# Kernel tuning notes

Hardware: AMD Instinct MI355X
Metric: run time of the kernel (lower is better)

## Reference

```python
import jax, jax.numpy as jnp
import numpy as np

U, I, H, E, EL = 100000, 50000, 128, 600000, 200000


def setup_inputs() -> dict:
    key = jax.random.key(0)
    ks = jax.random.split(key, 24)
    inp = {}
    inp["user_emb"] = jax.random.normal(ks[0], (U, H), jnp.float32) * 0.1
    inp["item_emb"] = jax.random.normal(ks[1], (I, H), jnp.float32) * 0.1
    s = 1.0 / np.sqrt(H)
    names = ["w1_ui_l", "w1_ui_r", "w1_iu_l", "w1_iu_r",
             "w2_ui_l", "w2_ui_r", "w2_iu_l", "w2_iu_r"]
    for i, n in enumerate(names):
        inp[n] = jax.random.uniform(ks[2 + i], (H, H), jnp.float32, -s, s)
    for i, n in enumerate(["b1_ui", "b1_iu", "b2_ui", "b2_iu"]):
        inp[n] = jax.random.uniform(ks[10 + i], (H,), jnp.float32, -s, s)
    inp["user_node_id"] = jnp.arange(U, dtype=jnp.int32)
    inp["item_node_id"] = jnp.arange(I, dtype=jnp.int32)
    src_u = jax.random.randint(ks[14], (E,), 0, U, jnp.int32)
    dst_i = jax.random.randint(ks[15], (E,), 0, I, jnp.int32)
    inp["edge_index_ui"] = jnp.stack([src_u, dst_i])  # user -> item
    inp["edge_index_iu"] = jnp.stack([dst_i, src_u])  # item -> user (reverse)
    lu = jax.random.randint(ks[16], (EL,), 0, U, jnp.int32)
    li = jax.random.randint(ks[17], (EL,), 0, I, jnp.int32)
    inp["edge_label_index"] = jnp.stack([lu, li])
    return inp


def _sage(x_src, x_dst, edge_index, w_l, b_l, w_r, num_dst):
    # PyG SAGEConv: out = lin_l(mean_j x_src[j]) + lin_r(x_dst)
    src, dst = edge_index[0], edge_index[1]
    msg = x_src[src]                                   # [E, H] gather
    agg = jax.ops.segment_sum(msg, dst, num_segments=num_dst)
    cnt = jax.ops.segment_sum(jnp.ones((msg.shape[0],), msg.dtype), dst,
                              num_segments=num_dst)
    mean = agg / jnp.maximum(cnt, 1.0)[:, None]
    return mean @ w_l + b_l + x_dst @ w_r


def reference(user_emb, item_emb,
              w1_ui_l, w1_ui_r, w1_iu_l, w1_iu_r,
              w2_ui_l, w2_ui_r, w2_iu_l, w2_iu_r,
              b1_ui, b1_iu, b2_ui, b2_iu,
              user_node_id, item_node_id,
              edge_index_ui, edge_index_iu, edge_label_index):
    xu = user_emb[user_node_id]   # [U, H]
    xi = item_emb[item_node_id]   # [I, H]
    # layer 1 (hetero: each dst type aggregates from its single incoming relation)
    u1 = jax.nn.relu(_sage(xi, xu, edge_index_iu, w1_iu_l, b1_iu, w1_iu_r, U))
    i1 = jax.nn.relu(_sage(xu, xi, edge_index_ui, w1_ui_l, b1_ui, w1_ui_r, I))
    # layer 2
    u2 = _sage(i1, u1, edge_index_iu, w2_iu_l, b2_iu, w2_iu_r, U)
    i2 = _sage(u1, i1, edge_index_ui, w2_ui_l, b2_ui, w2_ui_r, I)
    # edge-indexed dot-product classifier
    fu = u2[edge_label_index[0]]  # [EL, H]
    fi = i2[edge_label_index[1]]  # [EL, H]
    return jnp.sum(fu * fi, axis=-1)
```

## Files before the change

kernel.cpp:

```cpp
#include <hip/hip_runtime.h>
#include <hip/hip_bf16.h>
#include <cstdio>

#define U_N 100000
#define I_N 50000
#define H_DIM 128
#define E_N 600000
#define EL_N 200000

#define EPB 2048
#define NBLK ((E_N + EPB - 1) / EPB)
#define SH_U 8
#define SH_I 7
#define NB_U ((U_N + 255) >> 8)
#define NB_I ((I_N + 127) >> 7)
#define LH_U (NB_U * NBLK)
#define LH_I (NB_I * NBLK)

#define NBLK_GU ((U_N + 127) / 128)
#define NBLK_GI ((I_N + 127) / 128)

typedef __attribute__((ext_vector_type(8))) short bh8;
typedef __attribute__((ext_vector_type(4))) float f32x4;
typedef __attribute__((ext_vector_type(8))) unsigned short u16x8;

__device__ inline unsigned short f2b(float f) {
  unsigned u = __builtin_bit_cast(unsigned, f);
  u += 0x7fffu + ((u >> 16) & 1u);
  return (unsigned short)(u >> 16);
}
__device__ inline float b2f(unsigned short h) {
  unsigned u = ((unsigned)h) << 16;
  return __builtin_bit_cast(float, u);
}

__global__ __launch_bounds__(256) void bin_hist(const int* __restrict__ dst,
                                                int* __restrict__ hist,
                                                int shift, int nbins) {
  __shared__ int h[512];
  const int t = threadIdx.x;
  for (int i = t; i < nbins; i += 256) h[i] = 0;
  __syncthreads();
  const int base = blockIdx.x * EPB;
  const int end = min(base + EPB, E_N);
  for (int i = base + t; i < end; i += 256)
    atomicAdd(&h[((unsigned)dst[i]) >> shift], 1);
  __syncthreads();
  for (int i = t; i < nbins; i += 256)
    hist[i * NBLK + blockIdx.x] = h[i];
}

__global__ __launch_bounds__(256) void bin_scatter(const int* __restrict__ dst,
                                                   const int* __restrict__ src,
                                                   const int* __restrict__ hoff,
                                                   unsigned* __restrict__ bucketed,
                                                   int shift, int nbins) {
  __shared__ int cur[512];
  const int t = threadIdx.x;
  for (int i = t; i < nbins; i += 256) cur[i] = hoff[i * NBLK + blockIdx.x];
  __syncthreads();
  const int base = blockIdx.x * EPB;
  const int end = min(base + EPB, E_N);
  const unsigned mask = (1u << shift) - 1u;
  for (int i = base + t; i < end; i += 256) {
    unsigned d = (unsigned)dst[i];
    int bin = (int)(d >> shift);
    int pos = atomicAdd(&cur[bin], 1);
    bucketed[pos] = ((d & mask) << 24) | (unsigned)src[i];
  }
}

__global__ __launch_bounds__(256) void bin_group(const int* __restrict__ hoff,
                                                 const unsigned* __restrict__ bucketed,
                                                 int* __restrict__ csr,
                                                 int* __restrict__ cnt,
                                                 int* __restrict__ off,
                                                 int shift, int nbins, int N) {
  __shared__ int cl[256];
  __shared__ int cur[256];
  __shared__ int wsum[4];
  const int b = blockIdx.x;
  const int t = threadIdx.x;
  const int start = hoff[b * NBLK];
  const int end = (b + 1 < nbins) ? hoff[(b + 1) * NBLK] : E_N;
  const int ndst = 1 << shift;
  const int base = b << shift;
  if (t < ndst) cl[t] = 0;
  __syncthreads();
  for (int i = start + t; i < end; i += 256)
    atomicAdd(&cl[bucketed[i] >> 24], 1);
  __syncthreads();
  int v = (t < ndst) ? cl[t] : 0;
  const int lane = t & 63, wv = t >> 6;
  int inc = v;
  for (int d = 1; d < 64; d <<= 1) {
    int x = __shfl_up(inc, d, 64);
    if (lane >= d) inc += x;
  }
  if (lane == 63) wsum[wv] = inc;
  __syncthreads();
  int wbase = 0;
  for (int q = 0; q < wv; ++q) wbase += wsum[q];
  int excl = wbase + inc - v;
  if (t < ndst) {
    cur[t] = start + excl;
    int node = base + t;
    if (node < N) { cnt[node] = v; off[node] = start + excl; }
  }
  __syncthreads();
  for (int i = start + t; i < end; i += 256) {
    unsigned w = bucketed[i];
    int pos = atomicAdd(&cur[w >> 24], 1);
    csr[pos] = (int)(w & 0xFFFFFFu);
  }
}

__global__ __launch_bounds__(256) void cvt_emb2(const float* __restrict__ xu,
                                                const float* __restrict__ xi,
                                                const int* __restrict__ unid,
                                                const int* __restrict__ inid,
                                                unsigned short* __restrict__ ub,
                                                unsigned short* __restrict__ ib) {
  int t = blockIdx.x * 256 + threadIdx.x;
  const float* x;
  unsigned short* xb;
  int row, seg;
  if (t < U_N * 16) {
    row = t >> 4; seg = t & 15;
    row = unid ? unid[row] : row;
    x = xu; xb = ub + ((size_t)(t >> 4)) * H_DIM;
  } else {
    int t2 = t - U_N * 16;
    if (t2 >= I_N * 16) return;
    row = t2 >> 4; seg = t2 & 15;
    int r0 = row;
    row = inid ? inid[row] : row;
    x = xi; xb = ib + (size_t)r0 * H_DIM;
  }
  const float* p = x + (size_t)row * H_DIM + seg * 8;
  float4 a = ((const float4*)p)[0];
  float4 b = ((const float4*)p)[1];
  u16x8 v;
  v[0] = f2b(a.x); v[1] = f2b(a.y); v[2] = f2b(a.z); v[3] = f2b(a.w);
  v[4] = f2b(b.x); v[5] = f2b(b.y); v[6] = f2b(b.z); v[7] = f2b(b.w);
  *(u16x8*)(xb + seg * 8) = v;
}

__global__ __launch_bounds__(256) void scan_p1(const int* __restrict__ cnt,
                                               int* __restrict__ bsum, int n) {
  const int t = threadIdx.x;
  const int base = blockIdx.x * 1024 + t * 4;
  int s = 0;
  for (int j = 0; j < 4; ++j) {
    int i = base + j;
    if (i < n) s += cnt[i];
  }
  for (int off = 32; off > 0; off >>= 1) s += __shfl_down(s, off, 64);
  __shared__ int wsum[4];
  if ((t & 63) == 0) wsum[t >> 6] = s;
  __syncthreads();
  if (t == 0) bsum[blockIdx.x] = wsum[0] + wsum[1] + wsum[2] + wsum[3];
}

__global__ __launch_bounds__(256) void scan_p2(int* __restrict__ bsum, int nb) {
  __shared__ int sm[256];
  const int t = threadIdx.x;
  int v = (t < nb) ? bsum[t] : 0;
  sm[t] = v;
  __syncthreads();
  for (int d = 1; d < 256; d <<= 1) {
    int x = (t >= d) ? sm[t - d] : 0;
    __syncthreads();
    sm[t] += x;
    __syncthreads();
  }
  if (t < nb) bsum[t] = sm[t] - v;
}

__global__ __launch_bounds__(256) void scan_p3(const int* __restrict__ cnt,
                                               const int* __restrict__ bsum,
                                               int* __restrict__ off, int n) {
  const int t = threadIdx.x;
  const int lane = t & 63, wv = t >> 6;
  const int base = blockIdx.x * 1024 + t * 4;
  int vals[4];
  int s = 0;
  for (int j = 0; j < 4; ++j) {
    int i = base + j;
    vals[j] = (i < n) ? cnt[i] : 0;
    s += vals[j];
  }
  int inc = s;
  for (int d = 1; d < 64; d <<= 1) {
    int x = __shfl_up(inc, d, 64);
    if (lane >= d) inc += x;
  }
  __shared__ int wsum[4];
  if (lane == 63) wsum[wv] = inc;
  __syncthreads();
  int wbase = 0;
  for (int w = 0; w < wv; ++w) wbase += wsum[w];
  int excl = wbase + (inc - s) + bsum[blockIdx.x];
  for (int j = 0; j < 4; ++j) {
    int i = base + j;
    if (i < n) off[i] = excl;
    excl += vals[j];
  }
}

__global__ __launch_bounds__(256) void gather_mean2(
    const int* __restrict__ off_u, const int* __restrict__ cnt_u,
    const int* __restrict__ csr_u, const unsigned short* __restrict__ xsrc_u,
    unsigned short* __restrict__ agg_u,
    const int* __restrict__ off_i, const int* __restrict__ cnt_i,
    const int* __restrict__ csr_i, const unsigned short* __restrict__ xsrc_i,
    unsigned short* __restrict__ agg_i) {
  long t = (long)blockIdx.x * 256 + threadIdx.x;
  int node = (int)(t >> 4);
  int lane = (int)(t & 15);
  const int* off; const int* cnt; const int* csr;
  const unsigned short* xb; unsigned short* aggb;
  if (node < U_N) {
    off = off_u; cnt = cnt_u; csr = csr_u; xb = xsrc_u; aggb = agg_u;
  } else {
    node -= U_N;
    if (node >= I_N) return;
    off = off_i; cnt = cnt_i; csr = csr_i; xb = xsrc_i; aggb = agg_i;
  }
  int o = off[node], c = cnt[node];
  float acc[8] = {};
  for (int j0 = 0; j0 < c; j0 += 16) {
    int nj = c - j0;
    if (nj > 16) nj = 16;
    int sidx = (lane < nj) ? csr[o + j0 + lane] : 0;
    int j = 0;
    for (; j + 4 <= nj; j += 4) {
      int s0 = __shfl(sidx, j + 0, 16);
      int s1 = __shfl(sidx, j + 1, 16);
      int s2 = __shfl(sidx, j + 2, 16);
      int s3 = __shfl(sidx, j + 3, 16);
      u16x8 v0 = *(const u16x8*)(xb + (size_t)s0 * H_DIM + lane * 8);
      u16x8 v1 = *(const u16x8*)(xb + (size_t)s1 * H_DIM + lane * 8);
      u16x8 v2 = *(const u16x8*)(xb + (size_t)s2 * H_DIM + lane * 8);
      u16x8 v3 = *(const u16x8*)(xb + (size_t)s3 * H_DIM + lane * 8);
      for (int k = 0; k < 8; ++k) acc[k] += b2f(v0[k]);
      for (int k = 0; k < 8; ++k) acc[k] += b2f(v1[k]);
      for (int k = 0; k < 8; ++k) acc[k] += b2f(v2[k]);
      for (int k = 0; k < 8; ++k) acc[k] += b2f(v3[k]);
    }
    for (; j < nj; ++j) {
      int s = __shfl(sidx, j, 16);
      u16x8 v = *(const u16x8*)(xb + (size_t)s * H_DIM + lane * 8);
      for (int k = 0; k < 8; ++k) acc[k] += b2f(v[k]);
    }
  }
  float inv = 1.0f / (float)(c > 0 ? c : 1);
  u16x8 r;
  for (int k = 0; k < 8; ++k) r[k] = f2b(acc[k] * inv);
  *(u16x8*)(aggb + (size_t)node * H_DIM + lane * 8) = r;
}

__global__ __launch_bounds__(256) void prep_w4(
    const float* __restrict__ l0, const float* __restrict__ r0, short* __restrict__ o0,
    const float* __restrict__ l1, const float* __restrict__ r1, short* __restrict__ o1,
    const float* __restrict__ l2, const float* __restrict__ r2, short* __restrict__ o2,
    const float* __restrict__ l3, const float* __restrict__ r3, short* __restrict__ o3) {
  int t = blockIdx.x * 256 + threadIdx.x;
  int set = t >> 15, s = t & 32767;
  const float *wl, *wr; short* W2;
  if (set == 0)      { wl = l0; wr = r0; W2 = o0; }
  else if (set == 1) { wl = l1; wr = r1; W2 = o1; }
  else if (set == 2) { wl = l2; wr = r2; W2 = o2; }
  else               { wl = l3; wr = r3; W2 = o3; }
  int col = s >> 8, k = s & 255;
  float v = (k < 128) ? wl[k * 128 + col] : wr[(k - 128) * 128 + col];
  W2[col * 256 + k] = (short)f2b(v);
}

__global__ __launch_bounds__(256) void sage_gemm2(
    const unsigned short* __restrict__ agg_u, const unsigned short* __restrict__ x_u,
    const short* __restrict__ W2_u, const float* __restrict__ bias_u,
    unsigned short* __restrict__ out_u,
    const unsigned short* __restrict__ agg_i, const unsigned short* __restrict__ x_i,
    const short* __restrict__ W2_i, const float* __restrict__ bias_i,
    unsigned short* __restrict__ out_i, int relu) {
  const unsigned short *aggb, *xb;
  const short* W2;
  const float* bias;
  unsigned short* outb;
  int N, blk;
  if (blockIdx.x < NBLK_GU) {
    aggb = agg_u; xb = x_u; W2 = W2_u; bias = bias_u; outb = out_u;
    N = U_N; blk = blockIdx.x;
  } else {
    aggb = agg_i; xb = x_i; W2 = W2_i; bias = bias_i; outb = out_i;
    N = I_N; blk = blockIdx.x - NBLK_GU;
  }

  __shared__ short wlds[128 * 256];
  const int tid = threadIdx.x;
  for (int c = tid; c < 4096; c += 256) {
    int col = c >> 5, g = c & 31;
    uint4 v = *(const uint4*)(W2 + col * 256 + g * 8);
    *(uint4*)(&wlds[col * 256 + ((g ^ (col & 15)) * 8)]) = v;
  }
  __syncthreads();

  const int lane = tid & 63;
  const int wave = tid >> 6;
  const int q = lane >> 4;
  const int n16 = lane & 15;
  const int rowbase = blk * 128 + wave * 32;

  const unsigned short* aptr[2];
  const unsigned short* xptr[2];
  for (int g = 0; g < 2; ++g) {
    int row = rowbase + g * 16 + n16;
    int rr = row < N ? row : 0;
    aptr[g] = aggb + (size_t)rr * H_DIM + q * 8;
    xptr[g] = xb + (size_t)rr * H_DIM + q * 8;
  }

  f32x4 acc[2][8] = {};

  for (int kt = 0; kt < 8; ++kt) {
    const int k0 = kt * 32;
    bh8 afrag[2];
    for (int g = 0; g < 2; ++g) {
      const unsigned short* p = (kt < 4) ? (aptr[g] + k0) : (xptr[g] + (k0 - 128));
      afrag[g] = *(const bh8*)(p);
    }
    const int swz = ((kt * 4 + q) ^ n16) * 8;
    for (int c = 0; c < 8; ++c) {
      bh8 b = *(const bh8*)(&wlds[(c * 16 + n16) * 256 + swz]);
      acc[0][c] = __builtin_amdgcn_mfma_f32_16x16x32_bf16(afrag[0], b, acc[0][c], 0, 0, 0);
      acc[1][c] = __builtin_amdgcn_mfma_f32_16x16x32_bf16(afrag[1], b, acc[1][c], 0, 0, 0);
    }
  }

  float bcol[8];
  for (int c = 0; c < 8; ++c) bcol[c] = bias[c * 16 + n16];

  for (int g = 0; g < 2; ++g) {
    for (int r = 0; r < 4; ++r) {
      int row = rowbase + g * 16 + q * 4 + r;
      if (row >= N) continue;
      for (int c = 0; c < 8; ++c) {
        float v = acc[g][c][r] + bcol[c];
        if (relu) v = v > 0.0f ? v : 0.0f;
        outb[(size_t)row * H_DIM + c * 16 + n16] = f2b(v);
      }
    }
  }
}

__global__ __launch_bounds__(256) void final_dot(const int* __restrict__ lbl,
                                                 const unsigned short* __restrict__ u2,
                                                 const unsigned short* __restrict__ i2,
                                                 float* __restrict__ out) {
  long t = (long)blockIdx.x * 256 + threadIdx.x;
  int e = (int)(t >> 4);
  if (e >= EL_N) return;
  int lane = (int)(t & 15);
  int lu = lbl[e];
  int li = lbl[EL_N + e];
  u16x8 a = *(const u16x8*)(u2 + (size_t)lu * H_DIM + lane * 8);
  u16x8 b = *(const u16x8*)(i2 + (size_t)li * H_DIM + lane * 8);
  float p = 0.f;
  for (int k = 0; k < 8; ++k) p += b2f(a[k]) * b2f(b[k]);
  for (int off = 8; off > 0; off >>= 1) p += __shfl_down(p, off, 16);
  if (lane == 0) out[e] = p;
}

extern "C" void kernel_launch(void* const* d_in, const int* in_sizes, int n_in,
                              void* d_out, int out_size, void* d_ws, size_t ws_size,
                              hipStream_t stream) {
  const float* user_emb = (const float*)d_in[0];
  const float* item_emb = (const float*)d_in[1];
  const float* w1_ui_l = (const float*)d_in[2];
  const float* w1_ui_r = (const float*)d_in[3];
  const float* w1_iu_l = (const float*)d_in[4];
  const float* w1_iu_r = (const float*)d_in[5];
  const float* w2_ui_l = (const float*)d_in[6];
  const float* w2_ui_r = (const float*)d_in[7];
  const float* w2_iu_l = (const float*)d_in[8];
  const float* w2_iu_r = (const float*)d_in[9];
  const float* b1_ui = (const float*)d_in[10];
  const float* b1_iu = (const float*)d_in[11];
  const float* b2_ui = (const float*)d_in[12];
  const float* b2_iu = (const float*)d_in[13];
  const int* unid = (const int*)d_in[14];
  const int* inid = (const int*)d_in[15];
  const int* e_ui = (const int*)d_in[16];
  const int* e_iu = (const int*)d_in[17];
  const int* elbl = (const int*)d_in[18];
  float* out = (float*)d_out;

  char* ws = (char*)d_ws;
  size_t o = 0;
  auto alloc = [&](size_t bytes) {
    char* p = ws + o;
    o = (o + bytes + 255) & ~(size_t)255;
    return p;
  };
  int* hist_u = (int*)alloc((size_t)LH_U * 4);
  int* hoff_u = (int*)alloc((size_t)LH_U * 4);
  int* hist_i = (int*)alloc((size_t)LH_I * 4);
  int* hoff_i = (int*)alloc((size_t)LH_I * 4);
  unsigned* bkt_u = (unsigned*)alloc((size_t)E_N * 4);
  unsigned* bkt_i = (unsigned*)alloc((size_t)E_N * 4);
  int* cnt_u = (int*)alloc((size_t)U_N * 4);
  int* cnt_i = (int*)alloc((size_t)I_N * 4);
  int* off_u = (int*)alloc((size_t)U_N * 4);
  int* off_i = (int*)alloc((size_t)I_N * 4);
  int* csr_u = (int*)alloc((size_t)E_N * 4);
  int* csr_i = (int*)alloc((size_t)E_N * 4);
  int* bsum_u = (int*)alloc(256 * 4);
  int* bsum_i = (int*)alloc(256 * 4);
  unsigned short* ue_b = (unsigned short*)alloc((size_t)U_N * H_DIM * 2);
  unsigned short* ie_b = (unsigned short*)alloc((size_t)I_N * H_DIM * 2);
  unsigned short* agg_u = (unsigned short*)alloc((size_t)U_N * H_DIM * 2);
  unsigned short* agg_i = (unsigned short*)alloc((size_t)I_N * H_DIM * 2);
  unsigned short* h1_u = (unsigned short*)alloc((size_t)U_N * H_DIM * 2);
  unsigned short* h1_i = (unsigned short*)alloc((size_t)I_N * H_DIM * 2);
  unsigned short* h2_u = (unsigned short*)alloc((size_t)U_N * H_DIM * 2);
  unsigned short* h2_i = (unsigned short*)alloc((size_t)I_N * H_DIM * 2);
  short* W2_1u = (short*)alloc(128 * 256 * 2);
  short* W2_1i = (short*)alloc(128 * 256 * 2);
  short* W2_2u = (short*)alloc(128 * 256 * 2);
  short* W2_2i = (short*)alloc(128 * 256 * 2);
  if (o > ws_size) {
    fprintf(stderr, "kernel_launch: ws too small, need %zu have %zu\n", o, ws_size);
    return;
  }

  cvt_emb2<<<((U_N + I_N) * 16 + 255) / 256, 256, 0, stream>>>(
      user_emb, item_emb, unid, inid, ue_b, ie_b);
  prep_w4<<<512, 256, 0, stream>>>(w1_iu_l, w1_iu_r, W2_1u,
                                   w1_ui_l, w1_ui_r, W2_1i,
                                   w2_iu_l, w2_iu_r, W2_2u,
                                   w2_ui_l, w2_ui_r, W2_2i);

  bin_hist<<<NBLK, 256, 0, stream>>>(e_ui, hist_u, SH_U, NB_U);
  bin_hist<<<NBLK, 256, 0, stream>>>(e_ui + E_N, hist_i, SH_I, NB_I);

  scan_p1<<<(LH_U + 1023) / 1024, 256, 0, stream>>>(hist_u, bsum_u, LH_U);
  scan_p1<<<(LH_I + 1023) / 1024, 256, 0, stream>>>(hist_i, bsum_i, LH_I);
  scan_p2<<<1, 256, 0, stream>>>(bsum_u, (LH_U + 1023) / 1024);
  scan_p2<<<1, 256, 0, stream>>>(bsum_i, (LH_I + 1023) / 1024);
  scan_p3<<<(LH_U + 1023) / 1024, 256, 0, stream>>>(hist_u, bsum_u, hoff_u, LH_U);
  scan_p3<<<(LH_I + 1023) / 1024, 256, 0, stream>>>(hist_i, bsum_i, hoff_i, LH_I);

  bin_scatter<<<NBLK, 256, 0, stream>>>(e_ui, e_ui + E_N, hoff_u, bkt_u, SH_U, NB_U);
  bin_scatter<<<NBLK, 256, 0, stream>>>(e_ui + E_N, e_ui, hoff_i, bkt_i, SH_I, NB_I);

  bin_group<<<NB_U, 256, 0, stream>>>(hoff_u, bkt_u, csr_u, cnt_u, off_u, SH_U, NB_U, U_N);
  bin_group<<<NB_I, 256, 0, stream>>>(hoff_i, bkt_i, csr_i, cnt_i, off_i, SH_I, NB_I, I_N);

  const int g_blocks = ((U_N + I_N) * 16 + 255) / 256;
  gather_mean2<<<g_blocks, 256, 0, stream>>>(off_u, cnt_u, csr_u, ie_b, agg_u,
                                             off_i, cnt_i, csr_i, ue_b, agg_i);
  sage_gemm2<<<NBLK_GU + NBLK_GI, 256, 0, stream>>>(
      agg_u, ue_b, W2_1u, b1_iu, h1_u,
      agg_i, ie_b, W2_1i, b1_ui, h1_i, 1);

  gather_mean2<<<g_blocks, 256, 0, stream>>>(off_u, cnt_u, csr_u, h1_i, agg_u,
                                             off_i, cnt_i, csr_i, h1_u, agg_i);
  sage_gemm2<<<NBLK_GU + NBLK_GI, 256, 0, stream>>>(
      agg_u, h1_u, W2_2u, b2_iu, h2_u,
      agg_i, h1_i, W2_2i, b2_ui, h2_i, 0);

  final_dot<<<(EL_N * 16 + 255) / 256, 256, 0, stream>>>(elbl, h2_u, h2_i, out);
}
```

Baseline: 391.7 us.

## Merge preprocessing launches, unify CSR build, widen GEMM tiles, deepen gather unroll

Folds the embedding conversion, weight packing and both edge histograms into a single launch. The user and item CSR builds now share one buffer, so one scan chain and one scatter and group pass each replace the paired launches. The SAGE GEMM tile grows from 128 to 256 rows per block, with four row groups per wave and launch bounds allowing two blocks per CU. The neighbor gather adds an 8-way unrolled load loop to keep more loads in flight. The goal is fewer launches and serial gaps and more memory parallelism, at the cost of higher register pressure in the GEMM and fewer blocks for it.

```diff
diff --git a/kernel.cpp b/kernel.cpp
--- a/kernel.cpp
+++ b/kernel.cpp
@@ -16,9 +16,12 @@
 #define NB_I ((I_N + 127) >> 7)
 #define LH_U (NB_U * NBLK)
 #define LH_I (NB_I * NBLK)
-
-#define NBLK_GU ((U_N + 127) / 128)
-#define NBLK_GI ((I_N + 127) / 128)
+#define LH_TOT (LH_U + LH_I)
+
+#define CVT_BLK (((U_N + I_N) * 16) / 256)
+#define PREP_BLK 512
+#define NBU2 ((U_N + 255) / 256)
+#define NBI2 ((I_N + 255) / 256)
 
 typedef __attribute__((ext_vector_type(8))) short bh8;
 typedef __attribute__((ext_vector_type(4))) float f32x4;
@@ -34,116 +37,71 @@
   return __builtin_bit_cast(float, u);
 }
 
-__global__ __launch_bounds__(256) void bin_hist(const int* __restrict__ dst,
-                                                int* __restrict__ hist,
-                                                int shift, int nbins) {
+__global__ __launch_bounds__(256) void prep_all(
+    const float* __restrict__ xu, const float* __restrict__ xi,
+    const int* __restrict__ unid, const int* __restrict__ inid,
+    unsigned short* __restrict__ ub, unsigned short* __restrict__ ib,
+    const float* __restrict__ l0, const float* __restrict__ r0, short* __restrict__ o0,
+    const float* __restrict__ l1, const float* __restrict__ r1, short* __restrict__ o1,
+    const float* __restrict__ l2, const float* __restrict__ r2, short* __restrict__ o2,
+    const float* __restrict__ l3, const float* __restrict__ r3, short* __restrict__ o3,
+    const int* __restrict__ e_ui, int* __restrict__ hist) {
   __shared__ int h[512];
-  const int t = threadIdx.x;
-  for (int i = t; i < nbins; i += 256) h[i] = 0;
-  __syncthreads();
-  const int base = blockIdx.x * EPB;
-  const int end = min(base + EPB, E_N);
-  for (int i = base + t; i < end; i += 256)
-    atomicAdd(&h[((unsigned)dst[i]) >> shift], 1);
-  __syncthreads();
-  for (int i = t; i < nbins; i += 256)
-    hist[i * NBLK + blockIdx.x] = h[i];
-}
-
-__global__ __launch_bounds__(256) void bin_scatter(const int* __restrict__ dst,
-                                                   const int* __restrict__ src,
-                                                   const int* __restrict__ hoff,
-                                                   unsigned* __restrict__ bucketed,
-                                                   int shift, int nbins) {
-  __shared__ int cur[512];
-  const int t = threadIdx.x;
-  for (int i = t; i < nbins; i += 256) cur[i] = hoff[i * NBLK + blockIdx.x];
-  __syncthreads();
-  const int base = blockIdx.x * EPB;
-  const int end = min(base + EPB, E_N);
-  const unsigned mask = (1u << shift) - 1u;
-  for (int i = base + t; i < end; i += 256) {
-    unsigned d = (unsigned)dst[i];
-    int bin = (int)(d >> shift);
-    int pos = atomicAdd(&cur[bin], 1);
-    bucketed[pos] = ((d & mask) << 24) | (unsigned)src[i];
-  }
-}
-
-__global__ __launch_bounds__(256) void bin_group(const int* __restrict__ hoff,
-                                                 const unsigned* __restrict__ bucketed,
-                                                 int* __restrict__ csr,
-                                                 int* __restrict__ cnt,
-                                                 int* __restrict__ off,
-                                                 int shift, int nbins, int N) {
-  __shared__ int cl[256];
-  __shared__ int cur[256];
-  __shared__ int wsum[4];
   const int b = blockIdx.x;
-  const int t = threadIdx.x;
-  const int start = hoff[b * NBLK];
-  const int end = (b + 1 < nbins) ? hoff[(b + 1) * NBLK] : E_N;
-  const int ndst = 1 << shift;
-  const int base = b << shift;
-  if (t < ndst) cl[t] = 0;
-  __syncthreads();
-  for (int i = start + t; i < end; i += 256)
-    atomicAdd(&cl[bucketed[i] >> 24], 1);
-  __syncthreads();
-  int v = (t < ndst) ? cl[t] : 0;
-  const int lane = t & 63, wv = t >> 6;
-  int inc = v;
-  for (int d = 1; d < 64; d <<= 1) {
-    int x = __shfl_up(inc, d, 64);
-    if (lane >= d) inc += x;
-  }
-  if (lane == 63) wsum[wv] = inc;
-  __syncthreads();
-  int wbase = 0;
-  for (int q = 0; q < wv; ++q) wbase += wsum[q];
-  int excl = wbase + inc - v;
-  if (t < ndst) {
-    cur[t] = start + excl;
-    int node = base + t;
-    if (node < N) { cnt[node] = v; off[node] = start + excl; }
-  }
-  __syncthreads();
-  for (int i = start + t; i < end; i += 256) {
-    unsigned w = bucketed[i];
-    int pos = atomicAdd(&cur[w >> 24], 1);
-    csr[pos] = (int)(w & 0xFFFFFFu);
-  }
-}
-
-__global__ __launch_bounds__(256) void cvt_emb2(const float* __restrict__ xu,
-                                                const float* __restrict__ xi,
-                                                const int* __restrict__ unid,
-                                                const int* __restrict__ inid,
-                                                unsigned short* __restrict__ ub,
-                                                unsigned short* __restrict__ ib) {
-  int t = blockIdx.x * 256 + threadIdx.x;
-  const float* x;
-  unsigned short* xb;
-  int row, seg;
-  if (t < U_N * 16) {
-    row = t >> 4; seg = t & 15;
-    row = unid ? unid[row] : row;
-    x = xu; xb = ub + ((size_t)(t >> 4)) * H_DIM;
+  const int tid = threadIdx.x;
+  if (b < CVT_BLK) {
+    int t = b * 256 + tid;
+    const float* x;
+    unsigned short* xb;
+    int row, seg;
+    if (t < U_N * 16) {
+      row = t >> 4; seg = t & 15;
+      int r0_ = row;
+      row = unid ? unid[row] : row;
+      x = xu; xb = ub + (size_t)r0_ * H_DIM;
+    } else {
+      int t2 = t - U_N * 16;
+      row = t2 >> 4; seg = t2 & 15;
+      int r0_ = row;
+      row = inid ? inid[row] : row;
+      x = xi; xb = ib + (size_t)r0_ * H_DIM;
+    }
+    const float* p = x + (size_t)row * H_DIM + seg * 8;
+    float4 a = ((const float4*)p)[0];
+    float4 c = ((const float4*)p)[1];
+    u16x8 v;
+    v[0] = f2b(a.x); v[1] = f2b(a.y); v[2] = f2b(a.z); v[3] = f2b(a.w);
+    v[4] = f2b(c.x); v[5] = f2b(c.y); v[6] = f2b(c.z); v[7] = f2b(c.w);
+    *(u16x8*)(xb + seg * 8) = v;
+  } else if (b < CVT_BLK + PREP_BLK) {
+    int t = (b - CVT_BLK) * 256 + tid;
+    int set = t >> 15, s = t & 32767;
+    const float *wl, *wr; short* W2;
+    if (set == 0)      { wl = l0; wr = r0; W2 = o0; }
+    else if (set == 1) { wl = l1; wr = r1; W2 = o1; }
+    else if (set == 2) { wl = l2; wr = r2; W2 = o2; }
+    else               { wl = l3; wr = r3; W2 = o3; }
+    int col = s >> 8, k = s & 255;
+    float v = (k < 128) ? wl[k * 128 + col] : wr[(k - 128) * 128 + col];
+    W2[col * 256 + k] = (short)f2b(v);
   } else {
-    int t2 = t - U_N * 16;
-    if (t2 >= I_N * 16) return;
-    row = t2 >> 4; seg = t2 & 15;
-    int r0 = row;
-    row = inid ? inid[row] : row;
-    x = xi; xb = ib + (size_t)r0 * H_DIM;
-  }
-  const float* p = x + (size_t)row * H_DIM + seg * 8;
-  float4 a = ((const float4*)p)[0];
-  float4 b = ((const float4*)p)[1];
-  u16x8 v;
-  v[0] = f2b(a.x); v[1] = f2b(a.y); v[2] = f2b(a.z); v[3] = f2b(a.w);
-  v[4] = f2b(b.x); v[5] = f2b(b.y); v[6] = f2b(b.z); v[7] = f2b(b.w);
-  *(u16x8*)(xb + seg * 8) = v;
+    int hb = b - CVT_BLK - PREP_BLK;
+    int side = hb >= NBLK;
+    int blk = side ? hb - NBLK : hb;
+    const int* dst = e_ui + (side ? E_N : 0);
+    int shift = side ? SH_I : SH_U;
+    int nbins = side ? NB_I : NB_U;
+    int hbase = side ? LH_U : 0;
+    for (int i = tid; i < nbins; i += 256) h[i] = 0;
+    __syncthreads();
+    const int base = blk * EPB;
+    const int end = min(base + EPB, E_N);
+    for (int i = base + tid; i < end; i += 256)
+      atomicAdd(&h[((unsigned)dst[i]) >> shift], 1);
+    __syncthreads();
+    for (int i = tid; i < nbins; i += 256)
+      hist[hbase + i * NBLK + blk] = h[i];
+  }
 }
 
 __global__ __launch_bounds__(256) void scan_p1(const int* __restrict__ cnt,
@@ -208,24 +166,107 @@
   }
 }
 
+__global__ __launch_bounds__(256) void bin_scatter2(const int* __restrict__ e_ui,
+                                                    const int* __restrict__ hoff,
+                                                    unsigned* __restrict__ bucketed) {
+  __shared__ int cur[512];
+  const int t = threadIdx.x;
+  const int hb = blockIdx.x;
+  const int side = hb >= NBLK;
+  const int blk = side ? hb - NBLK : hb;
+  const int* dst = e_ui + (side ? E_N : 0);
+  const int* src = e_ui + (side ? 0 : E_N);
+  const int shift = side ? SH_I : SH_U;
+  const int nbins = side ? NB_I : NB_U;
+  const int hbase = side ? LH_U : 0;
+  for (int i = t; i < nbins; i += 256) cur[i] = hoff[hbase + i * NBLK + blk];
+  __syncthreads();
+  const int base = blk * EPB;
+  const int end = min(base + EPB, E_N);
+  const unsigned mask = (1u << shift) - 1u;
+  for (int i = base + t; i < end; i += 256) {
+    unsigned d = (unsigned)dst[i];
+    int bin = (int)(d >> shift);
+    int pos = atomicAdd(&cur[bin], 1);
+    bucketed[pos] = ((d & mask) << 24) | (unsigned)src[i];
+  }
+}
+
+__global__ __launch_bounds__(256) void bin_group2(const int* __restrict__ hoff,
+                                                  const unsigned* __restrict__ bucketed,
+                                                  int* __restrict__ csr,
+                                                  int* __restrict__ cnt_u,
+                                                  int* __restrict__ off_u,
+                                                  int* __restrict__ cnt_i,
+                                                  int* __restrict__ off_i) {
+  __shared__ int cl[256];
+  __shared__ int cur[256];
+  __shared__ int wsum[4];
+  const int b = blockIdx.x;
+  const int t = threadIdx.x;
+  const int side = b >= NB_U;
+  const int bb = side ? b - NB_U : b;
+  const int shift = side ? SH_I : SH_U;
+  const int N = side ? I_N : U_N;
+  int* cnt = side ? cnt_i : cnt_u;
+  int* off = side ? off_i : off_u;
+  int start, end;
+  if (!side) {
+    start = hoff[bb * NBLK];
+    end = (bb + 1 < NB_U) ? hoff[(bb + 1) * NBLK] : E_N;
+  } else {
+    start = hoff[LH_U + bb * NBLK];
+    end = (bb + 1 < NB_I) ? hoff[LH_U + (bb + 1) * NBLK] : 2 * E_N;
+  }
+  const int ndst = 1 << shift;
+  const int base = bb << shift;
+  if (t < ndst) cl[t] = 0;
+  __syncthreads();
+  for (int i = start + t; i < end; i += 256)
+    atomicAdd(&cl[bucketed[i] >> 24], 1);
+  __syncthreads();
+  int v = (t < ndst) ? cl[t] : 0;
+  const int lane = t & 63, wv = t >> 6;
+  int inc = v;
+  for (int d = 1; d < 64; d <<= 1) {
+    int x = __shfl_up(inc, d, 64);
+    if (lane >= d) inc += x;
+  }
+  if (lane == 63) wsum[wv] = inc;
+  __syncthreads();
+  int wbase = 0;
+  for (int q = 0; q < wv; ++q) wbase += wsum[q];
+  int excl = wbase + inc - v;
+  if (t < ndst) {
+    cur[t] = start + excl;
+    int node = base + t;
+    if (node < N) { cnt[node] = v; off[node] = start + excl; }
+  }
+  __syncthreads();
+  for (int i = start + t; i < end; i += 256) {
+    unsigned w = bucketed[i];
+    int pos = atomicAdd(&cur[w >> 24], 1);
+    csr[pos] = (int)(w & 0xFFFFFFu);
+  }
+}
+
 __global__ __launch_bounds__(256) void gather_mean2(
     const int* __restrict__ off_u, const int* __restrict__ cnt_u,
-    const int* __restrict__ csr_u, const unsigned short* __restrict__ xsrc_u,
-    unsigned short* __restrict__ agg_u,
+    const unsigned short* __restrict__ xsrc_u, unsigned short* __restrict__ agg_u,
     const int* __restrict__ off_i, const int* __restrict__ cnt_i,
-    const int* __restrict__ csr_i, const unsigned short* __restrict__ xsrc_i,
-    unsigned short* __restrict__ agg_i) {
+    const unsigned short* __restrict__ xsrc_i, unsigned short* __restrict__ agg_i,
+    const int* __restrict__ csr) {
   long t = (long)blockIdx.x * 256 + threadIdx.x;
   int node = (int)(t >> 4);
   int lane = (int)(t & 15);
-  const int* off; const int* cnt; const int* csr;
+  const int* off; const int* cnt;
   const unsigned short* xb; unsigned short* aggb;
   if (node < U_N) {
-    off = off_u; cnt = cnt_u; csr = csr_u; xb = xsrc_u; aggb = agg_u;
+    off = off_u; cnt = cnt_u; xb = xsrc_u; aggb = agg_u;
   } else {
     node -= U_N;
     if (node >= I_N) return;
-    off = off_i; cnt = cnt_i; csr = csr_i; xb = xsrc_i; aggb = agg_i;
+    off = off_i; cnt = cnt_i; xb = xsrc_i; aggb = agg_i;
   }
   int o = off[node], c = cnt[node];
   float acc[8] = {};
@@ -234,19 +275,23 @@
     if (nj > 16) nj = 16;
     int sidx = (lane < nj) ? csr[o + j0 + lane] : 0;
     int j = 0;
+    for (; j + 8 <= nj; j += 8) {
+      u16x8 v[8];
+      for (int m = 0; m < 8; ++m) {
+        int s = __shfl(sidx, j + m, 16);
+        v[m] = *(const u16x8*)(xb + (size_t)s * H_DIM + lane * 8);
+      }
+      for (int m = 0; m < 8; ++m)
+        for (int k = 0; k < 8; ++k) acc[k] += b2f(v[m][k]);
+    }
     for (; j + 4 <= nj; j += 4) {
-      int s0 = __shfl(sidx, j + 0, 16);
-      int s1 = __shfl(sidx, j + 1, 16);
-      int s2 = __shfl(sidx, j + 2, 16);
-      int s3 = __shfl(sidx, j + 3, 16);
-      u16x8 v0 = *(const u16x8*)(xb + (size_t)s0 * H_DIM + lane * 8);
-      u16x8 v1 = *(const u16x8*)(xb + (size_t)s1 * H_DIM + lane * 8);
-      u16x8 v2 = *(const u16x8*)(xb + (size_t)s2 * H_DIM + lane * 8);
-      u16x8 v3 = *(const u16x8*)(xb + (size_t)s3 * H_DIM + lane * 8);
-      for (int k = 0; k < 8; ++k) acc[k] += b2f(v0[k]);
-      for (int k = 0; k < 8; ++k) acc[k] += b2f(v1[k]);
-      for (int k = 0; k < 8; ++k) acc[k] += b2f(v2[k]);
-      for (int k = 0; k < 8; ++k) acc[k] += b2f(v3[k]);
+      u16x8 v[4];
+      for (int m = 0; m < 4; ++m) {
+        int s = __shfl(sidx, j + m, 16);
+        v[m] = *(const u16x8*)(xb + (size_t)s * H_DIM + lane * 8);
+      }
+      for (int m = 0; m < 4; ++m)
+        for (int k = 0; k < 8; ++k) acc[k] += b2f(v[m][k]);
     }
     for (; j < nj; ++j) {
       int s = __shfl(sidx, j, 16);
@@ -260,24 +305,7 @@
   *(u16x8*)(aggb + (size_t)node * H_DIM + lane * 8) = r;
 }
 
-__global__ __launch_bounds__(256) void prep_w4(
-    const float* __restrict__ l0, const float* __restrict__ r0, short* __restrict__ o0,
-    const float* __restrict__ l1, const float* __restrict__ r1, short* __restrict__ o1,
-    const float* __restrict__ l2, const float* __restrict__ r2, short* __restrict__ o2,
-    const float* __restrict__ l3, const float* __restrict__ r3, short* __restrict__ o3) {
-  int t = blockIdx.x * 256 + threadIdx.x;
-  int set = t >> 15, s = t & 32767;
-  const float *wl, *wr; short* W2;
-  if (set == 0)      { wl = l0; wr = r0; W2 = o0; }
-  else if (set == 1) { wl = l1; wr = r1; W2 = o1; }
-  else if (set == 2) { wl = l2; wr = r2; W2 = o2; }
-  else               { wl = l3; wr = r3; W2 = o3; }
-  int col = s >> 8, k = s & 255;
-  float v = (k < 128) ? wl[k * 128 + col] : wr[(k - 128) * 128 + col];
-  W2[col * 256 + k] = (short)f2b(v);
-}
-
-__global__ __launch_bounds__(256) void sage_gemm2(
+__global__ __launch_bounds__(256, 2) void sage_gemm2(
     const unsigned short* __restrict__ agg_u, const unsigned short* __restrict__ x_u,
     const short* __restrict__ W2_u, const float* __restrict__ bias_u,
     unsigned short* __restrict__ out_u,
@@ -289,12 +317,12 @@
   const float* bias;
   unsigned short* outb;
   int N, blk;
-  if (blockIdx.x < NBLK_GU) {
+  if (blockIdx.x < NBU2) {
     aggb = agg_u; xb = x_u; W2 = W2_u; bias = bias_u; outb = out_u;
     N = U_N; blk = blockIdx.x;
   } else {
     aggb = agg_i; xb = x_i; W2 = W2_i; bias = bias_i; outb = out_i;
-    N = I_N; blk = blockIdx.x - NBLK_GU;
+    N = I_N; blk = blockIdx.x - NBU2;
   }
 
   __shared__ short wlds[128 * 256];
@@ -310,23 +338,23 @@
   const int wave = tid >> 6;
   const int q = lane >> 4;
   const int n16 = lane & 15;
-  const int rowbase = blk * 128 + wave * 32;
-
-  const unsigned short* aptr[2];
-  const unsigned short* xptr[2];
-  for (int g = 0; g < 2; ++g) {
+  const int rowbase = blk * 256 + wave * 64;
+
+  const unsigned short* aptr[4];
+  const unsigned short* xptr[4];
+  for (int g = 0; g < 4; ++g) {
     int row = rowbase + g * 16 + n16;
     int rr = row < N ? row : 0;
     aptr[g] = aggb + (size_t)rr * H_DIM + q * 8;
     xptr[g] = xb + (size_t)rr * H_DIM + q * 8;
   }
 
-  f32x4 acc[2][8] = {};
+  f32x4 acc[4][8] = {};
 
   for (int kt = 0; kt < 8; ++kt) {
     const int k0 = kt * 32;
-    bh8 afrag[2];
-    for (int g = 0; g < 2; ++g) {
+    bh8 afrag[4];
+    for (int g = 0; g < 4; ++g) {
       const unsigned short* p = (kt < 4) ? (aptr[g] + k0) : (xptr[g] + (k0 - 128));
       afrag[g] = *(const bh8*)(p);
     }
@@ -335,13 +363,15 @@
       bh8 b = *(const bh8*)(&wlds[(c * 16 + n16) * 256 + swz]);
       acc[0][c] = __builtin_amdgcn_mfma_f32_16x16x32_bf16(afrag[0], b, acc[0][c], 0, 0, 0);
       acc[1][c] = __builtin_amdgcn_mfma_f32_16x16x32_bf16(afrag[1], b, acc[1][c], 0, 0, 0);
+      acc[2][c] = __builtin_amdgcn_mfma_f32_16x16x32_bf16(afrag[2], b, acc[2][c], 0, 0, 0);
+      acc[3][c] = __builtin_amdgcn_mfma_f32_16x16x32_bf16(afrag[3], b, acc[3][c], 0, 0, 0);
     }
   }
 
   float bcol[8];
   for (int c = 0; c < 8; ++c) bcol[c] = bias[c * 16 + n16];
 
-  for (int g = 0; g < 2; ++g) {
+  for (int g = 0; g < 4; ++g) {
     for (int r = 0; r < 4; ++r) {
       int row = rowbase + g * 16 + q * 4 + r;
       if (row >= N) continue;
@@ -403,20 +433,15 @@
     o = (o + bytes + 255) & ~(size_t)255;
     return p;
   };
-  int* hist_u = (int*)alloc((size_t)LH_U * 4);
-  int* hoff_u = (int*)alloc((size_t)LH_U * 4);
-  int* hist_i = (int*)alloc((size_t)LH_I * 4);
-  int* hoff_i = (int*)alloc((size_t)LH_I * 4);
-  unsigned* bkt_u = (unsigned*)alloc((size_t)E_N * 4);
-  unsigned* bkt_i = (unsigned*)alloc((size_t)E_N * 4);
+  int* hist = (int*)alloc((size_t)LH_TOT * 4);
+  int* hoff = (int*)alloc((size_t)LH_TOT * 4);
+  unsigned* bkt = (unsigned*)alloc((size_t)2 * E_N * 4);
+  int* csr = (int*)alloc((size_t)2 * E_N * 4);
   int* cnt_u = (int*)alloc((size_t)U_N * 4);
   int* cnt_i = (int*)alloc((size_t)I_N * 4);
   int* off_u = (int*)alloc((size_t)U_N * 4);
   int* off_i = (int*)alloc((size_t)I_N * 4);
-  int* csr_u = (int*)alloc((size_t)E_N * 4);
-  int* csr_i = (int*)alloc((size_t)E_N * 4);
-  int* bsum_u = (int*)alloc(256 * 4);
-  int* bsum_i = (int*)alloc(256 * 4);
+  int* bsum = (int*)alloc(256 * 4);
   unsigned short* ue_b = (unsigned short*)alloc((size_t)U_N * H_DIM * 2);
   unsigned short* ie_b = (unsigned short*)alloc((size_t)I_N * H_DIM * 2);
   unsigned short* agg_u = (unsigned short*)alloc((size_t)U_N * H_DIM * 2);
@@ -434,39 +459,30 @@
     return;
   }
 
-  cvt_emb2<<<((U_N + I_N) * 16 + 255) / 256, 256, 0, stream>>>(
-      user_emb, item_emb, unid, inid, ue_b, ie_b);
-  prep_w4<<<512, 256, 0, stream>>>(w1_iu_l, w1_iu_r, W2_1u,
-                                   w1_ui_l, w1_ui_r, W2_1i,
-                                   w2_iu_l, w2_iu_r, W2_2u,
-                                   w2_ui_l, w2_ui_r, W2_2i);
-
-  bin_hist<<<NBLK, 256, 0, stream>>>(e_ui, hist_u, SH_U, NB_U);
-  bin_hist<<<NBLK, 256, 0, stream>>>(e_ui + E_N, hist_i, SH_I, NB_I);
-
-  scan_p1<<<(LH_U + 1023) / 1024, 256, 0, stream>>>(hist_u, bsum_u, LH_U);
-  scan_p1<<<(LH_I + 1023) / 1024, 256, 0, stream>>>(hist_i, bsum_i, LH_I);
-  scan_p2<<<1, 256, 0, stream>>>(bsum_u, (LH_U + 1023) / 1024);
-  scan_p2<<<1, 256, 0, stream>>>(bsum_i, (LH_I + 1023) / 1024);
-  scan_p3<<<(LH_U + 1023) / 1024, 256, 0, stream>>>(hist_u, bsum_u, hoff_u, LH_U);
-  scan_p3<<<(LH_I + 1023) / 1024, 256, 0, stream>>>(hist_i, bsum_i, hoff_i, LH_I);
-
-  bin_scatter<<<NBLK, 256, 0, stream>>>(e_ui, e_ui + E_N, hoff_u, bkt_u, SH_U, NB_U);
-  bin_scatter<<<NBLK, 256, 0, stream>>>(e_ui + E_N, e_ui, hoff_i, bkt_i, SH_I, NB_I);
-
-  bin_group<<<NB_U, 256, 0, stream>>>(hoff_u, bkt_u, csr_u, cnt_u, off_u, SH_U, NB_U, U_N);
-  bin_group<<<NB_I, 256, 0, stream>>>(hoff_i, bkt_i, csr_i, cnt_i, off_i, SH_I, NB_I, I_N);
+  prep_all<<<CVT_BLK + PREP_BLK + 2 * NBLK, 256, 0, stream>>>(
+      user_emb, item_emb, unid, inid, ue_b, ie_b,
+      w1_iu_l, w1_iu_r, W2_1u, w1_ui_l, w1_ui_r, W2_1i,
+      w2_iu_l, w2_iu_r, W2_2u, w2_ui_l, w2_ui_r, W2_2i,
+      e_ui, hist);
+
+  const int nb1 = (LH_TOT + 1023) / 1024;
+  scan_p1<<<nb1, 256, 0, stream>>>(hist, bsum, LH_TOT);
+  scan_p2<<<1, 256, 0, stream>>>(bsum, nb1);
+  scan_p3<<<nb1, 256, 0, stream>>>(hist, bsum, hoff, LH_TOT);
+
+  bin_scatter2<<<2 * NBLK, 256, 0, stream>>>(e_ui, hoff, bkt);
+  bin_group2<<<NB_U + NB_I, 256, 0, stream>>>(hoff, bkt, csr, cnt_u, off_u, cnt_i, off_i);
 
   const int g_blocks = ((U_N + I_N) * 16 + 255) / 256;
-  gather_mean2<<<g_blocks, 256, 0, stream>>>(off_u, cnt_u, csr_u, ie_b, agg_u,
-                                             off_i, cnt_i, csr_i, ue_b, agg_i);
-  sage_gemm2<<<NBLK_GU + NBLK_GI, 256, 0, stream>>>(
+  gather_mean2<<<g_blocks, 256, 0, stream>>>(off_u, cnt_u, ie_b, agg_u,
+                                             off_i, cnt_i, ue_b, agg_i, csr);
+  sage_gemm2<<<NBU2 + NBI2, 256, 0, stream>>>(
       agg_u, ue_b, W2_1u, b1_iu, h1_u,
       agg_i, ie_b, W2_1i, b1_ui, h1_i, 1);
 
-  gather_mean2<<<g_blocks, 256, 0, stream>>>(off_u, cnt_u, csr_u, h1_i, agg_u,
-                                             off_i, cnt_i, csr_i, h1_u, agg_i);
-  sage_gemm2<<<NBLK_GU + NBLK_GI, 256, 0, stream>>>(
+  gather_mean2<<<g_blocks, 256, 0, stream>>>(off_u, cnt_u, h1_i, agg_u,
+                                             off_i, cnt_i, h1_u, agg_i, csr);
+  sage_gemm2<<<NBU2 + NBI2, 256, 0, stream>>>(
       agg_u, h1_u, W2_2u, b2_iu, h2_u,
       agg_i, h1_i, W2_2i, b2_ui, h2_i, 0);
 
```

After: 361.9 us. 1.08x faster.
